# Performance work log

Measured on AMD Instinct MI355X. Metric: run time of the kernel, lower is better.

The kernel has to match this reference:

```python
import jax, jax.numpy as jnp
import numpy as np

N_NODES = 100000
N_FEATURES = 512
N_HIDDEN = 256
N_EDGES = 3200000


def setup_inputs() -> dict:
    key = jax.random.key(0)
    k_x, k_r, k_c, k_v, k_w, k_b = jax.random.split(key, 6)
    x = jax.random.normal(k_x, (1, N_NODES, N_FEATURES), dtype=jnp.float32)
    adj_rows = jax.random.randint(k_r, (N_EDGES,), 0, N_NODES, dtype=jnp.int32)
    adj_cols = jax.random.randint(k_c, (N_EDGES,), 0, N_NODES, dtype=jnp.int32)
    adj_vals = jax.random.uniform(k_v, (N_EDGES,), dtype=jnp.float32)
    # Linear params: xavier_normal_ on weight [H, F], default bias init
    std = float(np.sqrt(2.0 / (N_FEATURES + N_HIDDEN)))
    W = jax.random.normal(k_w, (N_HIDDEN, N_FEATURES), dtype=jnp.float32) * std
    bound = float(1.0 / np.sqrt(N_FEATURES))
    b = jax.random.uniform(k_b, (N_HIDDEN,), dtype=jnp.float32, minval=-bound, maxval=bound)
    alpha = jnp.asarray(0.25, dtype=jnp.float32)  # PReLU default single-param init
    return {"x": x, "adj_rows": adj_rows, "adj_cols": adj_cols,
            "adj_vals": adj_vals, "W": W, "b": b, "alpha": alpha}


def reference(x, adj_rows, adj_cols, adj_vals, W, b, alpha):
    # Linear: [1, N, F] @ [F, H] + [H] -> squeeze to [N, H]
    h = (jnp.einsum('bnf,hf->bnh', x, W) + b)[0]
    # spmm(adj, h): gather source rows, scale by edge value, scatter-add to dest rows
    msgs = adj_vals[:, None] * h[adj_cols]              # [E, H]
    agg = jax.ops.segment_sum(msgs, adj_rows, num_segments=N_NODES)  # [N, H]
    out = jnp.where(agg >= 0, agg, alpha * agg)         # PReLU
    return out[None]                                     # [1, N, H]
```

## Files before the change

### kernel.cpp

```cpp
#include <hip/hip_runtime.h>


#define K_DIM 512
#define H_DIM 256

#define BIN_ROWS 512
#define NBIN_MAX 256
#define EB 18432
#define P1_CHUNK 4096
#define P1_PER_T 16

typedef __attribute__((ext_vector_type(8))) short short8;
typedef __attribute__((ext_vector_type(4))) float floatx4;

__device__ inline short f32_to_bf16(float f) {
    unsigned u = __float_as_uint(f);
    u += 0x7fffu + ((u >> 16) & 1u);
    return (short)(u >> 16);
}
__device__ inline float bf16_to_f32(unsigned short u) {
    return __uint_as_float(((unsigned)u) << 16);
}

#define GT_M 128
#define GT_N 256
#define GT_K 32
#define LDSW 32

__global__ __launch_bounds__(256, 2) void gemm_bf16_kernel(
    const float* __restrict__ A,
    const float* __restrict__ W,
    const float* __restrict__ bias,
    unsigned short* __restrict__ H,
    int M)
{
    __shared__ short As[GT_M * LDSW];
    __shared__ short Bs[GT_N * LDSW];

    const int tid  = threadIdx.x;
    const int m0   = blockIdx.x * GT_M;

    const int wave = tid >> 6;
    const int lane = tid & 63;
    const int wm   = (wave & 1) * 64;
    const int wn   = (wave >> 1) * 128;
    const int quad = lane >> 4;
    const int l16  = lane & 15;

    const int srow  = tid >> 1;
    const int shalf = tid & 1;

    floatx4 acc[4][8] = {};

    for (int k0 = 0; k0 < K_DIM; k0 += GT_K) {
        {
            int gm = m0 + srow;
            float f[16];
            if (gm < M) {
                const float* src = A + (size_t)gm * K_DIM + k0 + shalf * 16;
                *(float4*)(f + 0)  = *(const float4*)(src + 0);
                *(float4*)(f + 4)  = *(const float4*)(src + 4);
                *(float4*)(f + 8)  = *(const float4*)(src + 8);
                *(float4*)(f + 12) = *(const float4*)(src + 12);
            } else {
                #pragma unroll
                for (int j = 0; j < 16; ++j) f[j] = 0.f;
            }
            short8 v0, v1;
            #pragma unroll
            for (int j = 0; j < 8; ++j) { v0[j] = f32_to_bf16(f[j]); v1[j] = f32_to_bf16(f[8 + j]); }
            *(short8*)&As[srow * LDSW + shalf * 16 + 0] = v0;
            *(short8*)&As[srow * LDSW + shalf * 16 + 8] = v1;
        }
        #pragma unroll
        for (int it = 0; it < 2; ++it) {
            int gn = srow + it * 128;
            const float* src = W + (size_t)gn * K_DIM + k0 + shalf * 16;
            float f[16];
            *(float4*)(f + 0)  = *(const float4*)(src + 0);
            *(float4*)(f + 4)  = *(const float4*)(src + 4);
            *(float4*)(f + 8)  = *(const float4*)(src + 8);
            *(float4*)(f + 12) = *(const float4*)(src + 12);
            short8 v0, v1;
            #pragma unroll
            for (int j = 0; j < 8; ++j) { v0[j] = f32_to_bf16(f[j]); v1[j] = f32_to_bf16(f[8 + j]); }
            *(short8*)&Bs[gn * LDSW + shalf * 16 + 0] = v0;
            *(short8*)&Bs[gn * LDSW + shalf * 16 + 8] = v1;
        }
        __syncthreads();

        short8 af[4], bf[8];
        #pragma unroll
        for (int t = 0; t < 4; ++t)
            af[t] = *(const short8*)&As[(wm + t * 16 + l16) * LDSW + quad * 8];
        #pragma unroll
        for (int t = 0; t < 8; ++t)
            bf[t] = *(const short8*)&Bs[(wn + t * 16 + l16) * LDSW + quad * 8];
        #pragma unroll
        for (int i = 0; i < 4; ++i)
            #pragma unroll
            for (int j = 0; j < 8; ++j)
                acc[i][j] = __builtin_amdgcn_mfma_f32_16x16x32_bf16(af[i], bf[j], acc[i][j], 0, 0, 0);
        __syncthreads();
    }

    #pragma unroll
    for (int j = 0; j < 8; ++j) {
        int gcol = wn + j * 16 + l16;
        float bj = bias[gcol];
        #pragma unroll
        for (int i = 0; i < 4; ++i) {
            int rbase = m0 + wm + i * 16 + quad * 4;
            #pragma unroll
            for (int r = 0; r < 4; ++r) {
                int gm = rbase + r;
                if (gm < M)
                    H[(size_t)gm * H_DIM + gcol] =
                        (unsigned short)f32_to_bf16(acc[i][j][r] + bj);
            }
        }
    }
}

__global__ __launch_bounds__(256, 2) void partition_kernel(
    const int* __restrict__ rows, const int* __restrict__ cols,
    const float* __restrict__ vals, int* __restrict__ binCursor,
    int2* __restrict__ binned, int E, int nbins)
{
    __shared__ int hist[NBIN_MAX];
    __shared__ int binOff[NBIN_MAX];
    __shared__ int gbase[NBIN_MAX];
    __shared__ int cursor[NBIN_MAX];
    __shared__ int sc[2][NBIN_MAX];
    __shared__ int2 stage[P1_CHUNK];
    __shared__ unsigned char binOf[P1_CHUNK];

    const int tid = threadIdx.x;
    const int e0  = blockIdx.x * P1_CHUNK;
    const int total = min(P1_CHUNK, E - e0);

    int r[P1_PER_T], c[P1_PER_T];
    float v[P1_PER_T];
    #pragma unroll
    for (int i = 0; i < P1_PER_T; ++i) {
        int e = e0 + tid + i * 256;
        if (e < E) { r[i] = rows[e]; c[i] = cols[e]; v[i] = vals[e]; }
        else       { r[i] = -1; c[i] = 0; v[i] = 0.f; }
    }

    hist[tid] = 0;
    __syncthreads();
    #pragma unroll
    for (int i = 0; i < P1_PER_T; ++i)
        if (r[i] >= 0) atomicAdd(&hist[r[i] >> 9], 1);
    __syncthreads();

    int x = hist[tid];
    sc[0][tid] = x;
    __syncthreads();
    int cur = 0;
    for (int d = 1; d < 256; d <<= 1) {
        int y = sc[cur][tid];
        if (tid >= d) y += sc[cur][tid - d];
        sc[cur ^ 1][tid] = y;
        __syncthreads();
        cur ^= 1;
    }
    int excl = sc[cur][tid] - x;
    binOff[tid] = excl;
    cursor[tid] = excl;
    if (tid < nbins) gbase[tid] = atomicAdd(&binCursor[tid], x);
    else             gbase[tid] = 0;
    __syncthreads();

    #pragma unroll
    for (int i = 0; i < P1_PER_T; ++i) {
        if (r[i] >= 0) {
            int bin  = r[i] >> 9;
            int lpos = atomicAdd(&cursor[bin], 1);
            stage[lpos] = make_int2(((r[i] & (BIN_ROWS - 1)) << 17) | c[i],
                                    __float_as_int(v[i]));
            binOf[lpos] = (unsigned char)bin;
        }
    }
    __syncthreads();

    #pragma unroll
    for (int i = 0; i < P1_PER_T; ++i) {
        int idx = tid + i * 256;
        if (idx < total) {
            int bin = binOf[idx];
            int rel = gbase[bin] + (idx - binOff[bin]);
            if (rel < EB)
                binned[(size_t)bin * EB + rel] = stage[idx];
        }
    }
}

__global__ __launch_bounds__(512, 1) void binsort_kernel(
    const int2* __restrict__ binned, const int* __restrict__ binCursor,
    int2* __restrict__ sorted, int* __restrict__ rowstart,
    int* __restrict__ degArr, int M)
{
    __shared__ int hist[BIN_ROWS];
    __shared__ int cursor[BIN_ROWS];
    __shared__ int sc[2][BIN_ROWS];

    const int b   = blockIdx.x;
    const int tid = threadIdx.x;
    int cnt = binCursor[b]; if (cnt > EB) cnt = EB;
    int rows_here = M - b * BIN_ROWS; if (rows_here > BIN_ROWS) rows_here = BIN_ROWS;

    hist[tid] = 0;
    __syncthreads();
    const int2* src = binned + (size_t)b * EB;
    for (int i = tid; i < cnt; i += 512)
        atomicAdd(&hist[((unsigned)src[i].x) >> 17], 1);
    __syncthreads();

    int x = hist[tid];
    sc[0][tid] = x;
    __syncthreads();
    int cur = 0;
    for (int d = 1; d < 512; d <<= 1) {
        int y = sc[cur][tid];
        if (tid >= d) y += sc[cur][tid - d];
        sc[cur ^ 1][tid] = y;
        __syncthreads();
        cur ^= 1;
    }
    int excl = sc[cur][tid] - x;
    cursor[tid] = excl;
    if (tid < rows_here) {
        rowstart[b * BIN_ROWS + tid] = b * EB + excl;
        degArr[b * BIN_ROWS + tid]   = x;
    }
    __syncthreads();

    int2* dst = sorted + (size_t)b * EB;
    for (int i = tid; i < cnt; i += 512) {
        int2 p  = src[i];
        int rl  = ((unsigned)p.x) >> 17;
        int pos = atomicAdd(&cursor[rl], 1);
        dst[pos] = make_int2(p.x & 0x1FFFF, p.y);
    }
}

__global__ __launch_bounds__(256) void spmm_gather_kernel(
    const unsigned short* __restrict__ h, const int* __restrict__ rowstart,
    const int* __restrict__ degArr, const int2* __restrict__ sorted,
    const float* __restrict__ alpha_p, float* __restrict__ out, int M)
{
    const int wave = threadIdx.x >> 6;
    const int lane = threadIdx.x & 63;
    const int row = blockIdx.x * 4 + wave;
    if (row >= M) return;

    int deg = degArr[row];
    const int2* ep = sorted + rowstart[row];

    float4 acc = make_float4(0.f, 0.f, 0.f, 0.f);
    int e = 0;
    for (; e + 4 <= deg; e += 4) {
        int2 p0 = ep[e + 0];
        int2 p1 = ep[e + 1];
        int2 p2 = ep[e + 2];
        int2 p3 = ep[e + 3];
        ushort4 u0 = *(const ushort4*)(h + (size_t)p0.x * H_DIM + lane * 4);
        ushort4 u1 = *(const ushort4*)(h + (size_t)p1.x * H_DIM + lane * 4);
        ushort4 u2 = *(const ushort4*)(h + (size_t)p2.x * H_DIM + lane * 4);
        ushort4 u3 = *(const ushort4*)(h + (size_t)p3.x * H_DIM + lane * 4);
        float v0 = __int_as_float(p0.y);
        float v1 = __int_as_float(p1.y);
        float v2 = __int_as_float(p2.y);
        float v3 = __int_as_float(p3.y);
        acc.x += v0 * bf16_to_f32(u0.x); acc.y += v0 * bf16_to_f32(u0.y);
        acc.z += v0 * bf16_to_f32(u0.z); acc.w += v0 * bf16_to_f32(u0.w);
        acc.x += v1 * bf16_to_f32(u1.x); acc.y += v1 * bf16_to_f32(u1.y);
        acc.z += v1 * bf16_to_f32(u1.z); acc.w += v1 * bf16_to_f32(u1.w);
        acc.x += v2 * bf16_to_f32(u2.x); acc.y += v2 * bf16_to_f32(u2.y);
        acc.z += v2 * bf16_to_f32(u2.z); acc.w += v2 * bf16_to_f32(u2.w);
        acc.x += v3 * bf16_to_f32(u3.x); acc.y += v3 * bf16_to_f32(u3.y);
        acc.z += v3 * bf16_to_f32(u3.z); acc.w += v3 * bf16_to_f32(u3.w);
    }
    for (; e < deg; ++e) {
        int2 p = ep[e];
        ushort4 u = *(const ushort4*)(h + (size_t)p.x * H_DIM + lane * 4);
        float v = __int_as_float(p.y);
        acc.x += v * bf16_to_f32(u.x); acc.y += v * bf16_to_f32(u.y);
        acc.z += v * bf16_to_f32(u.z); acc.w += v * bf16_to_f32(u.w);
    }

    const float alpha = *alpha_p;
    acc.x = acc.x >= 0.f ? acc.x : alpha * acc.x;
    acc.y = acc.y >= 0.f ? acc.y : alpha * acc.y;
    acc.z = acc.z >= 0.f ? acc.z : alpha * acc.z;
    acc.w = acc.w >= 0.f ? acc.w : alpha * acc.w;
    *(float4*)(out + (size_t)row * H_DIM + lane * 4) = acc;
}

extern "C" void kernel_launch(void* const* d_in, const int* in_sizes, int n_in,
                              void* d_out, int out_size, void* d_ws, size_t ws_size,
                              hipStream_t stream) {
    const float* x        = (const float*)d_in[0];
    const int*   adj_rows = (const int*)d_in[1];
    const int*   adj_cols = (const int*)d_in[2];
    const float* adj_vals = (const float*)d_in[3];
    const float* W        = (const float*)d_in[4];
    const float* b        = (const float*)d_in[5];
    const float* alpha    = (const float*)d_in[6];
    float* out = (float*)d_out;

    const int M = in_sizes[0] / K_DIM;
    const int E = in_sizes[1];
    const int nbins = (M + BIN_ROWS - 1) / BIN_ROWS;

    char* ws = (char*)d_ws;
    size_t off = 0;
    auto alloc = [&](size_t bytes) {
        char* p = ws + off;
        off += (bytes + 255) & ~(size_t)255;
        return p;
    };
    unsigned short* h = (unsigned short*)alloc((size_t)M * H_DIM * sizeof(unsigned short));
    int2* binned  = (int2*)alloc((size_t)nbins * EB * sizeof(int2));
    int2* sorted  = (int2*)alloc((size_t)nbins * EB * sizeof(int2));
    int*  rowstart = (int*)alloc((size_t)M * sizeof(int));
    int*  degArr   = (int*)alloc((size_t)M * sizeof(int));
    int*  binCursor = (int*)alloc((size_t)NBIN_MAX * sizeof(int));

    gemm_bf16_kernel<<<dim3((M + GT_M - 1) / GT_M, 1), 256, 0, stream>>>(x, W, b, h, M);

    hipMemsetAsync(binCursor, 0, (size_t)NBIN_MAX * sizeof(int), stream);
    partition_kernel<<<(E + P1_CHUNK - 1) / P1_CHUNK, 256, 0, stream>>>(
        adj_rows, adj_cols, adj_vals, binCursor, binned, E, nbins);

    binsort_kernel<<<nbins, 512, 0, stream>>>(binned, binCursor, sorted,
                                              rowstart, degArr, M);

    spmm_gather_kernel<<<(M + 3) / 4, 256, 0, stream>>>(h, rowstart, degArr, sorted,
                                                        alpha, out, M);
}
```

Measured before the change: 673.0 us.

## Pre-convert W to bf16, widen partition/binsort blocks, pipeline SpMM gathers via shuffles

Adds a small kernel that converts W to bf16 once, so each GEMM block loads bf16 weights instead of re-converting fp32 per tile. Partition and binsort kernels now run with 1024-thread blocks (fewer elements per thread), with scan steps guarded by thread index. The SpMM gather loads 64 edge records per wave at once, broadcasts them with shuffles, and double-buffers 8 row gathers to raise memory-level parallelism. The cost is an extra launch and more register pressure in the gather loop.

```diff
diff --git a/kernel.cpp b/kernel.cpp
--- a/kernel.cpp
+++ b/kernel.cpp
@@ -8,7 +8,8 @@
 #define NBIN_MAX 256
 #define EB 18432
 #define P1_CHUNK 4096
-#define P1_PER_T 16
+#define P1_PER_T 4
+#define SPU 8
 
 typedef __attribute__((ext_vector_type(8))) short short8;
 typedef __attribute__((ext_vector_type(4))) float floatx4;
@@ -22,6 +23,20 @@
     return __uint_as_float(((unsigned)u) << 16);
 }
 
+__global__ __launch_bounds__(256) void convert_w_kernel(
+    const float* __restrict__ W, unsigned short* __restrict__ Wbf)
+{
+    int i = (blockIdx.x * 256 + threadIdx.x) * 8;
+    float4 a = *(const float4*)(W + i);
+    float4 b = *(const float4*)(W + i + 4);
+    short8 v;
+    v[0] = f32_to_bf16(a.x); v[1] = f32_to_bf16(a.y);
+    v[2] = f32_to_bf16(a.z); v[3] = f32_to_bf16(a.w);
+    v[4] = f32_to_bf16(b.x); v[5] = f32_to_bf16(b.y);
+    v[6] = f32_to_bf16(b.z); v[7] = f32_to_bf16(b.w);
+    *(short8*)((short*)Wbf + i) = v;
+}
+
 #define GT_M 128
 #define GT_N 256
 #define GT_K 32
@@ -29,7 +44,7 @@
 
 __global__ __launch_bounds__(256, 2) void gemm_bf16_kernel(
     const float* __restrict__ A,
-    const float* __restrict__ W,
+    const unsigned short* __restrict__ Wbf,
     const float* __restrict__ bias,
     unsigned short* __restrict__ H,
     int M)
@@ -75,15 +90,9 @@
         #pragma unroll
         for (int it = 0; it < 2; ++it) {
             int gn = srow + it * 128;
-            const float* src = W + (size_t)gn * K_DIM + k0 + shalf * 16;
-            float f[16];
-            *(float4*)(f + 0)  = *(const float4*)(src + 0);
-            *(float4*)(f + 4)  = *(const float4*)(src + 4);
-            *(float4*)(f + 8)  = *(const float4*)(src + 8);
-            *(float4*)(f + 12) = *(const float4*)(src + 12);
-            short8 v0, v1;
-            #pragma unroll
-            for (int j = 0; j < 8; ++j) { v0[j] = f32_to_bf16(f[j]); v1[j] = f32_to_bf16(f[8 + j]); }
+            const unsigned short* src = Wbf + (size_t)gn * K_DIM + k0 + shalf * 16;
+            short8 v0 = *(const short8*)(src + 0);
+            short8 v1 = *(const short8*)(src + 8);
             *(short8*)&Bs[gn * LDSW + shalf * 16 + 0] = v0;
             *(short8*)&Bs[gn * LDSW + shalf * 16 + 8] = v1;
         }
@@ -122,7 +131,7 @@
     }
 }
 
-__global__ __launch_bounds__(256, 2) void partition_kernel(
+__global__ __launch_bounds__(1024) void partition_kernel(
     const int* __restrict__ rows, const int* __restrict__ cols,
     const float* __restrict__ vals, int* __restrict__ binCursor,
     int2* __restrict__ binned, int E, int nbins)
@@ -143,34 +152,38 @@
     float v[P1_PER_T];
     #pragma unroll
     for (int i = 0; i < P1_PER_T; ++i) {
-        int e = e0 + tid + i * 256;
+        int e = e0 + tid + i * 1024;
         if (e < E) { r[i] = rows[e]; c[i] = cols[e]; v[i] = vals[e]; }
         else       { r[i] = -1; c[i] = 0; v[i] = 0.f; }
     }
 
-    hist[tid] = 0;
+    if (tid < NBIN_MAX) hist[tid] = 0;
     __syncthreads();
     #pragma unroll
     for (int i = 0; i < P1_PER_T; ++i)
         if (r[i] >= 0) atomicAdd(&hist[r[i] >> 9], 1);
     __syncthreads();
 
-    int x = hist[tid];
-    sc[0][tid] = x;
+    if (tid < NBIN_MAX) sc[0][tid] = hist[tid];
     __syncthreads();
     int cur = 0;
-    for (int d = 1; d < 256; d <<= 1) {
-        int y = sc[cur][tid];
-        if (tid >= d) y += sc[cur][tid - d];
-        sc[cur ^ 1][tid] = y;
+    for (int d = 1; d < NBIN_MAX; d <<= 1) {
+        if (tid < NBIN_MAX) {
+            int y = sc[cur][tid];
+            if (tid >= d) y += sc[cur][tid - d];
+            sc[cur ^ 1][tid] = y;
+        }
         __syncthreads();
         cur ^= 1;
     }
-    int excl = sc[cur][tid] - x;
-    binOff[tid] = excl;
-    cursor[tid] = excl;
-    if (tid < nbins) gbase[tid] = atomicAdd(&binCursor[tid], x);
-    else             gbase[tid] = 0;
+    if (tid < NBIN_MAX) {
+        int x    = hist[tid];
+        int excl = sc[cur][tid] - x;
+        binOff[tid] = excl;
+        cursor[tid] = excl;
+        if (tid < nbins) gbase[tid] = atomicAdd(&binCursor[tid], x);
+        else             gbase[tid] = 0;
+    }
     __syncthreads();
 
     #pragma unroll
@@ -187,7 +200,7 @@
 
     #pragma unroll
     for (int i = 0; i < P1_PER_T; ++i) {
-        int idx = tid + i * 256;
+        int idx = tid + i * 1024;
         if (idx < total) {
             int bin = binOf[idx];
             int rel = gbase[bin] + (idx - binOff[bin]);
@@ -197,7 +210,7 @@
     }
 }
 
-__global__ __launch_bounds__(512, 1) void binsort_kernel(
+__global__ __launch_bounds__(1024) void binsort_kernel(
     const int2* __restrict__ binned, const int* __restrict__ binCursor,
     int2* __restrict__ sorted, int* __restrict__ rowstart,
     int* __restrict__ degArr, int M)
@@ -211,34 +224,38 @@
     int cnt = binCursor[b]; if (cnt > EB) cnt = EB;
     int rows_here = M - b * BIN_ROWS; if (rows_here > BIN_ROWS) rows_here = BIN_ROWS;
 
-    hist[tid] = 0;
+    if (tid < BIN_ROWS) hist[tid] = 0;
     __syncthreads();
     const int2* src = binned + (size_t)b * EB;
-    for (int i = tid; i < cnt; i += 512)
+    for (int i = tid; i < cnt; i += 1024)
         atomicAdd(&hist[((unsigned)src[i].x) >> 17], 1);
     __syncthreads();
 
-    int x = hist[tid];
-    sc[0][tid] = x;
+    if (tid < BIN_ROWS) sc[0][tid] = hist[tid];
     __syncthreads();
     int cur = 0;
-    for (int d = 1; d < 512; d <<= 1) {
-        int y = sc[cur][tid];
-        if (tid >= d) y += sc[cur][tid - d];
-        sc[cur ^ 1][tid] = y;
+    for (int d = 1; d < BIN_ROWS; d <<= 1) {
+        if (tid < BIN_ROWS) {
+            int y = sc[cur][tid];
+            if (tid >= d) y += sc[cur][tid - d];
+            sc[cur ^ 1][tid] = y;
+        }
         __syncthreads();
         cur ^= 1;
     }
-    int excl = sc[cur][tid] - x;
-    cursor[tid] = excl;
-    if (tid < rows_here) {
-        rowstart[b * BIN_ROWS + tid] = b * EB + excl;
-        degArr[b * BIN_ROWS + tid]   = x;
+    if (tid < BIN_ROWS) {
+        int x    = hist[tid];
+        int excl = sc[cur][tid] - x;
+        cursor[tid] = excl;
+        if (tid < rows_here) {
+            rowstart[b * BIN_ROWS + tid] = b * EB + excl;
+            degArr[b * BIN_ROWS + tid]   = x;
+        }
     }
     __syncthreads();
 
     int2* dst = sorted + (size_t)b * EB;
-    for (int i = tid; i < cnt; i += 512) {
+    for (int i = tid; i < cnt; i += 1024) {
         int2 p  = src[i];
         int rl  = ((unsigned)p.x) >> 17;
         int pos = atomicAdd(&cursor[rl], 1);
@@ -256,39 +273,51 @@
     const int row = blockIdx.x * 4 + wave;
     if (row >= M) return;
 
-    int deg = degArr[row];
+    const int deg = degArr[row];
     const int2* ep = sorted + rowstart[row];
 
     float4 acc = make_float4(0.f, 0.f, 0.f, 0.f);
-    int e = 0;
-    for (; e + 4 <= deg; e += 4) {
-        int2 p0 = ep[e + 0];
-        int2 p1 = ep[e + 1];
-        int2 p2 = ep[e + 2];
-        int2 p3 = ep[e + 3];
-        ushort4 u0 = *(const ushort4*)(h + (size_t)p0.x * H_DIM + lane * 4);
-        ushort4 u1 = *(const ushort4*)(h + (size_t)p1.x * H_DIM + lane * 4);
-        ushort4 u2 = *(const ushort4*)(h + (size_t)p2.x * H_DIM + lane * 4);
-        ushort4 u3 = *(const ushort4*)(h + (size_t)p3.x * H_DIM + lane * 4);
-        float v0 = __int_as_float(p0.y);
-        float v1 = __int_as_float(p1.y);
-        float v2 = __int_as_float(p2.y);
-        float v3 = __int_as_float(p3.y);
-        acc.x += v0 * bf16_to_f32(u0.x); acc.y += v0 * bf16_to_f32(u0.y);
-        acc.z += v0 * bf16_to_f32(u0.z); acc.w += v0 * bf16_to_f32(u0.w);
-        acc.x += v1 * bf16_to_f32(u1.x); acc.y += v1 * bf16_to_f32(u1.y);
-        acc.z += v1 * bf16_to_f32(u1.z); acc.w += v1 * bf16_to_f32(u1.w);
-        acc.x += v2 * bf16_to_f32(u2.x); acc.y += v2 * bf16_to_f32(u2.y);
-        acc.z += v2 * bf16_to_f32(u2.z); acc.w += v2 * bf16_to_f32(u2.w);
-        acc.x += v3 * bf16_to_f32(u3.x); acc.y += v3 * bf16_to_f32(u3.y);
-        acc.z += v3 * bf16_to_f32(u3.z); acc.w += v3 * bf16_to_f32(u3.w);
-    }
-    for (; e < deg; ++e) {
-        int2 p = ep[e];
-        ushort4 u = *(const ushort4*)(h + (size_t)p.x * H_DIM + lane * 4);
-        float v = __int_as_float(p.y);
-        acc.x += v * bf16_to_f32(u.x); acc.y += v * bf16_to_f32(u.y);
-        acc.z += v * bf16_to_f32(u.z); acc.w += v * bf16_to_f32(u.w);
+
+    for (int chunk = 0; chunk < deg; chunk += 64) {
+        int rem = deg - chunk;
+        int n   = rem < 64 ? rem : 64;
+        int ru  = (n + SPU - 1) & ~(SPU - 1);
+        int2 p  = (chunk + lane < deg) ? ep[chunk + lane] : make_int2(0, 0);
+
+        ushort4 u[SPU]; float vv[SPU];
+        #pragma unroll
+        for (int j = 0; j < SPU; ++j) {
+            int c  = __shfl(p.x, j);
+            vv[j]  = __int_as_float(__shfl(p.y, j));
+            u[j]   = *(const ushort4*)(h + (size_t)c * H_DIM + lane * 4);
+        }
+        for (int e = SPU; e < ru; e += SPU) {
+            ushort4 u2[SPU]; float vv2[SPU];
+            #pragma unroll
+            for (int j = 0; j < SPU; ++j) {
+                int c   = __shfl(p.x, e + j);
+                vv2[j]  = __int_as_float(__shfl(p.y, e + j));
+                u2[j]   = *(const ushort4*)(h + (size_t)c * H_DIM + lane * 4);
+            }
+            #pragma unroll
+            for (int j = 0; j < SPU; ++j) {
+                float v = vv[j];
+                acc.x += v * bf16_to_f32(u[j].x);
+                acc.y += v * bf16_to_f32(u[j].y);
+                acc.z += v * bf16_to_f32(u[j].z);
+                acc.w += v * bf16_to_f32(u[j].w);
+            }
+            #pragma unroll
+            for (int j = 0; j < SPU; ++j) { u[j] = u2[j]; vv[j] = vv2[j]; }
+        }
+        #pragma unroll
+        for (int j = 0; j < SPU; ++j) {
+            float v = vv[j];
+            acc.x += v * bf16_to_f32(u[j].x);
+            acc.y += v * bf16_to_f32(u[j].y);
+            acc.z += v * bf16_to_f32(u[j].z);
+            acc.w += v * bf16_to_f32(u[j].w);
+        }
     }
 
     const float alpha = *alpha_p;
@@ -328,15 +357,18 @@
     int*  rowstart = (int*)alloc((size_t)M * sizeof(int));
     int*  degArr   = (int*)alloc((size_t)M * sizeof(int));
     int*  binCursor = (int*)alloc((size_t)NBIN_MAX * sizeof(int));
-
-    gemm_bf16_kernel<<<dim3((M + GT_M - 1) / GT_M, 1), 256, 0, stream>>>(x, W, b, h, M);
+    unsigned short* Wbf = (unsigned short*)alloc((size_t)H_DIM * K_DIM * sizeof(unsigned short));
+
+    convert_w_kernel<<<64, 256, 0, stream>>>(W, Wbf);
+
+    gemm_bf16_kernel<<<dim3((M + GT_M - 1) / GT_M, 1), 256, 0, stream>>>(x, Wbf, b, h, M);
 
     hipMemsetAsync(binCursor, 0, (size_t)NBIN_MAX * sizeof(int), stream);
-    partition_kernel<<<(E + P1_CHUNK - 1) / P1_CHUNK, 256, 0, stream>>>(
+    partition_kernel<<<(E + P1_CHUNK - 1) / P1_CHUNK, 1024, 0, stream>>>(
         adj_rows, adj_cols, adj_vals, binCursor, binned, E, nbins);
 
-    binsort_kernel<<<nbins, 512, 0, stream>>>(binned, binCursor, sorted,
-                                              rowstart, degArr, M);
+    binsort_kernel<<<nbins, 1024, 0, stream>>>(binned, binCursor, sorted,
+                                               rowstart, degArr, M);
 
     spmm_gather_kernel<<<(M + 3) / 4, 256, 0, stream>>>(h, rowstart, degArr, sorted,
                                                         alpha, out, M);
```

New measurement: 652.1 us. -3.1%, faster.
